# Performance work log

Hardware: AMD Instinct MI355X
Metric: run time of the kernel (lower is better)

The kernel has to match this reference:

```python
import jax, jax.numpy as jnp
import numpy as np

B = 128          # batch (stands in for bit-packed words)
C, H, W = 3, 32, 32
K = 64           # num_kernels
RFS, STRIDE = 5, 1
HO = (H - RFS) // STRIDE + 1   # 28
P = HO * HO                     # 784 output positions
G0 = 8                          # 2**tree_depth, tree_depth=3
NL1, NL2, NCLS = 64000, 32000, 10

# ALL_OPERATIONS order; each gate is multilinear: c0 + ca*a + cb*b + cab*a*b
COEF = jnp.array([
    [0, 0, 0, 0],    # zero
    [0, 0, 0, 1],    # and
    [0, 1, 0, -1],   # not_implies (a & ~b)
    [0, 1, 0, 0],    # a
    [0, 0, 1, -1],   # not_implied_by (b & ~a)
    [0, 0, 1, 0],    # b
    [0, 1, 1, -2],   # xor
    [0, 1, 1, -1],   # or
    [1, -1, -1, 1],  # not_or
    [1, -1, -1, 2],  # not_xor
    [1, 0, -1, 0],   # not_b
    [1, 0, -1, 1],   # implied_by (~b | a)
    [1, -1, 0, 0],   # not_a
    [1, -1, 0, 1],   # implies (~a | b)
    [1, 0, 0, -1],   # not_and
    [1, 0, 0, 0],    # one
], dtype=jnp.float32)


def _gate(a, b, ops):
    # ops: int array broadcastable against a/b trailing dims
    c = COEF[ops]  # [..., 4]
    return c[..., 0] + c[..., 1] * a + c[..., 2] * b + c[..., 3] * (a * b)


def _forward(x, cl, cr, o0, o1, o2, o3, a1, b1, p1, a2, b2, p2):
    # Conv logic layer: gather level-0 operand pairs -> [B, K, P, G0]
    la = jnp.take(x, cl, axis=1)
    lb = jnp.take(x, cr, axis=1)
    g = _gate(la, lb, o0[:, None, :])            # ops per (kernel, gate)
    # Binary tree reduction: level l pairs gates (2i, 2i+1)
    for ops in (o1, o2, o3):
        g = _gate(g[..., 0::2], g[..., 1::2], ops[:, None, :])
    z = g[..., 0].reshape(x.shape[0], K * P)     # [B, 50176]
    # Logic linear layers: out[i] = gate(in[a[i]], in[b[i]], op[i])
    z = _gate(z[:, a1], z[:, b1], p1)            # [B, NL1]
    z = _gate(z[:, a2], z[:, b2], p2)            # [B, NL2]
    # GroupSum: popcount per class group
    return z.reshape(z.shape[0], NCLS, -1).sum(-1)  # [B, 10]


def setup_inputs() -> dict:
    key = jax.random.key(0)
    x = (jax.random.uniform(key, (B, C * H * W)) < 0.5).astype(jnp.float32)
    rng = np.random.default_rng(0)
    bh = np.repeat(np.arange(HO), HO)  # h_pos per position
    bw = np.tile(np.arange(HO), HO)    # w_pos per position

    def conv_idx():
        dh = rng.integers(0, RFS, (K, P, G0))
        dw = rng.integers(0, RFS, (K, P, G0))
        dc = rng.integers(0, C, (K, P, G0))
        idx = dc * H * W + (bh[None, :, None] * STRIDE + dh) * W + (bw[None, :, None] * STRIDE + dw)
        return jnp.asarray(idx.astype(np.int32))

    ops = lambda shape: jnp.asarray(rng.integers(0, 16, shape).astype(np.int32))
    ridx = lambda hi, n: jnp.asarray(rng.integers(0, hi, n).astype(np.int32))
    return {
        'x': x,
        'conv_left_idx': conv_idx(), 'conv_right_idx': conv_idx(),
        'conv_ops0': ops((K, G0)), 'conv_ops1': ops((K, 4)),
        'conv_ops2': ops((K, 2)), 'conv_ops3': ops((K, 1)),
        'lin1_a': ridx(K * P, NL1), 'lin1_b': ridx(K * P, NL1), 'lin1_ops': ops((NL1,)),
        'lin2_a': ridx(NL1, NL2), 'lin2_b': ridx(NL1, NL2), 'lin2_ops': ops((NL2,)),
    }


def reference(x, conv_left_idx, conv_right_idx, conv_ops0, conv_ops1, conv_ops2, conv_ops3,
              lin1_a, lin1_b, lin1_ops, lin2_a, lin2_b, lin2_ops):
    return _forward(x, conv_left_idx, conv_right_idx, conv_ops0, conv_ops1, conv_ops2, conv_ops3,
                    lin1_a, lin1_b, lin1_ops, lin2_a, lin2_b, lin2_ops)
```

## Files before the change

### kernel.cpp

```cpp
#include <hip/hip_runtime.h>
#include <stdint.h>

#define NFEAT 3072
#define NWORD 2
#define NK 64
#define NP 784
#define NG 8
#define KP (NK * NP)
#define NL1 64000
#define NL2 32000
#define NCLS 10
#define NB 128
#define JBLK 128
#define CONV_THREADS 128

__device__ __forceinline__ uint64_t bsel64(uint64_t x, uint64_t p, uint64_t q) {
    return (x & p) | (~x & q);
}
__device__ __forceinline__ ulonglong2 gate128(ulonglong2 A, ulonglong2 B, int op) {
    uint64_t m3 = (uint64_t)0 - (uint64_t)((op >> 0) & 1);
    uint64_t m2 = (uint64_t)0 - (uint64_t)((op >> 1) & 1);
    uint64_t m1 = (uint64_t)0 - (uint64_t)((op >> 2) & 1);
    uint64_t m0 = (uint64_t)0 - (uint64_t)((op >> 3) & 1);
    ulonglong2 r;
    r.x = bsel64(A.x, bsel64(B.x, m3, m2), bsel64(B.x, m1, m0));
    r.y = bsel64(A.y, bsel64(B.y, m3, m2), bsel64(B.y, m1, m0));
    return r;
}

__global__ __launch_bounds__(256) void pack_kernel(const float* __restrict__ x,
                                                   uint64_t* __restrict__ xb,
                                                   float* __restrict__ out) {
    int gt = blockIdx.x * 256 + threadIdx.x;
    if (gt < NB * NCLS) out[gt] = 0.0f;
    int fw = gt >> 6;
    int lane = gt & 63;
    int f = fw >> 1, w = fw & 1;
    float val = x[(size_t)(w * 64 + lane) * NFEAT + f];
    uint64_t m = __ballot(val != 0.0f);
    if (lane == 0) xb[f * NWORD + w] = m;
}

__global__ __launch_bounds__(CONV_THREADS) void conv_kernel(
    const uint64_t* __restrict__ xb,
    const int* __restrict__ cl, const int* __restrict__ cr,
    const int* __restrict__ o0, const int* __restrict__ o1,
    const int* __restrict__ o2, const int* __restrict__ o3,
    uint64_t* __restrict__ z) {
    __shared__ uint64_t sxb[NFEAT * NWORD];
    {
        ulonglong2* s2 = reinterpret_cast<ulonglong2*>(sxb);
        const ulonglong2* g2 = reinterpret_cast<const ulonglong2*>(xb);
        for (int i = threadIdx.x; i < NFEAT; i += blockDim.x)
            s2[i] = g2[i];
    }
    __syncthreads();

    int t = blockIdx.x * CONV_THREADS + threadIdx.x;
    int k = t / NP;

    const int4* cl4 = reinterpret_cast<const int4*>(cl + (size_t)t * NG);
    const int4* cr4 = reinterpret_cast<const int4*>(cr + (size_t)t * NG);
    int4 l0 = cl4[0], l1 = cl4[1];
    int4 r0 = cr4[0], r1 = cr4[1];
    int la[NG] = {l0.x, l0.y, l0.z, l0.w, l1.x, l1.y, l1.z, l1.w};
    int rb[NG] = {r0.x, r0.y, r0.z, r0.w, r1.x, r1.y, r1.z, r1.w};

    int op0[NG], op1[4], op2[2], op3;
#pragma unroll
    for (int g = 0; g < NG; ++g) op0[g] = o0[k * NG + g];
#pragma unroll
    for (int g = 0; g < 4; ++g) op1[g] = o1[k * 4 + g];
#pragma unroll
    for (int g = 0; g < 2; ++g) op2[g] = o2[k * 2 + g];
    op3 = o3[k];

    const ulonglong2* sxb2 = reinterpret_cast<const ulonglong2*>(sxb);
    ulonglong2 gg[NG];
#pragma unroll
    for (int g = 0; g < NG; ++g) {
        ulonglong2 va = sxb2[la[g]];
        ulonglong2 vb = sxb2[rb[g]];
        gg[g] = gate128(va, vb, op0[g]);
    }
#pragma unroll
    for (int g = 0; g < 4; ++g)
        gg[g] = gate128(gg[2 * g], gg[2 * g + 1], op1[g]);
#pragma unroll
    for (int g = 0; g < 2; ++g)
        gg[g] = gate128(gg[2 * g], gg[2 * g + 1], op2[g]);
    reinterpret_cast<ulonglong2*>(z)[t] = gate128(gg[0], gg[1], op3);
}

__global__ __launch_bounds__(JBLK) void lin2_fused_kernel(
    const uint64_t* __restrict__ z,
    const int* __restrict__ a1, const int* __restrict__ b1,
    const int* __restrict__ p1,
    const int* __restrict__ a2, const int* __restrict__ b2,
    const int* __restrict__ p2, float* __restrict__ out) {
    __shared__ alignas(16) uint64_t s[NWORD][JBLK];
    int blk = blockIdx.x;
    const int chunks_per_cls = (NL2 / NCLS) / JBLK;
    int c = blk / chunks_per_cls;
    int j = c * (NL2 / NCLS) + (blk % chunks_per_cls) * JBLK + threadIdx.x;

    int ia = a2[j], ib = b2[j], op = p2[j];
    int iaa = a1[ia], iab = b1[ia], opa = p1[ia];
    int iba = a1[ib], ibb = b1[ib], opb = p1[ib];
    const ulonglong2* z2p = reinterpret_cast<const ulonglong2*>(z);
    ulonglong2 za = gate128(z2p[iaa], z2p[iab], opa);
    ulonglong2 zb = gate128(z2p[iba], z2p[ibb], opb);
    ulonglong2 zz = gate128(za, zb, op);
    s[0][threadIdx.x] = zz.x;
    s[1][threadIdx.x] = zz.y;
    __syncthreads();

    int bb = threadIdx.x;
    int w = bb >> 6, sh = bb & 63;
    const ulonglong2* sp = reinterpret_cast<const ulonglong2*>(s[w]);
    int cnt = 0;
#pragma unroll 16
    for (int jj = 0; jj < JBLK / 2; ++jj) {
        ulonglong2 v = sp[jj];
        cnt += (int)((v.x >> sh) & 1) + (int)((v.y >> sh) & 1);
    }
    atomicAdd(&out[bb * NCLS + c], (float)cnt);
}

extern "C" void kernel_launch(void* const* d_in, const int* in_sizes, int n_in,
                              void* d_out, int out_size, void* d_ws, size_t ws_size,
                              hipStream_t stream) {
    const float* x  = (const float*)d_in[0];
    const int* cl   = (const int*)d_in[1];
    const int* cr   = (const int*)d_in[2];
    const int* o0   = (const int*)d_in[3];
    const int* o1   = (const int*)d_in[4];
    const int* o2   = (const int*)d_in[5];
    const int* o3   = (const int*)d_in[6];
    const int* a1   = (const int*)d_in[7];
    const int* b1   = (const int*)d_in[8];
    const int* p1   = (const int*)d_in[9];
    const int* a2   = (const int*)d_in[10];
    const int* b2   = (const int*)d_in[11];
    const int* p2   = (const int*)d_in[12];
    float* out = (float*)d_out;

    uint8_t* ws = (uint8_t*)d_ws;
    uint64_t* xb = (uint64_t*)(ws);
    uint64_t* z  = (uint64_t*)(ws + 64 * 1024);

    pack_kernel<<<(NFEAT * NWORD * 64) / 256, 256, 0, stream>>>(x, xb, out);
    conv_kernel<<<KP / CONV_THREADS, CONV_THREADS, 0, stream>>>(xb, cl, cr, o0, o1, o2, o3, z);
    lin2_fused_kernel<<<NL2 / JBLK, JBLK, 0, stream>>>(z, a1, b1, p1, a2, b2, p2, out);
}
```

Measured before the change: 102.4 us.

## Fuse pack, conv and linear stages into one cooperative persistent kernel

```diff
diff --git a/kernel.cpp b/kernel.cpp
--- a/kernel.cpp
+++ b/kernel.cpp
@@ -1,5 +1,8 @@
 #include <hip/hip_runtime.h>
+#include <hip/hip_cooperative_groups.h>
 #include <stdint.h>
+
+namespace cg = cooperative_groups;
 
 #define NFEAT 3072
 #define NWORD 2
@@ -12,7 +15,9 @@
 #define NCLS 10
 #define NB 128
 #define JBLK 128
-#define CONV_THREADS 128
+#define GRID 256
+#define BLK 256
+#define ITEMS_PER_BLK (KP / GRID)
 
 __device__ __forceinline__ uint64_t bsel64(uint64_t x, uint64_t p, uint64_t q) {
     return (x & p) | (~x & q);
@@ -28,103 +33,112 @@
     return r;
 }
 
-__global__ __launch_bounds__(256) void pack_kernel(const float* __restrict__ x,
-                                                   uint64_t* __restrict__ xb,
-                                                   float* __restrict__ out) {
-    int gt = blockIdx.x * 256 + threadIdx.x;
-    if (gt < NB * NCLS) out[gt] = 0.0f;
-    int fw = gt >> 6;
-    int lane = gt & 63;
-    int f = fw >> 1, w = fw & 1;
-    float val = x[(size_t)(w * 64 + lane) * NFEAT + f];
-    uint64_t m = __ballot(val != 0.0f);
-    if (lane == 0) xb[f * NWORD + w] = m;
-}
-
-__global__ __launch_bounds__(CONV_THREADS) void conv_kernel(
-    const uint64_t* __restrict__ xb,
+__global__ __launch_bounds__(BLK) void fused_all(
+    const float* __restrict__ x,
     const int* __restrict__ cl, const int* __restrict__ cr,
     const int* __restrict__ o0, const int* __restrict__ o1,
     const int* __restrict__ o2, const int* __restrict__ o3,
-    uint64_t* __restrict__ z) {
-    __shared__ uint64_t sxb[NFEAT * NWORD];
+    const int* __restrict__ a1, const int* __restrict__ b1,
+    const int* __restrict__ p1,
+    const int* __restrict__ a2, const int* __restrict__ b2,
+    const int* __restrict__ p2,
+    uint64_t* __restrict__ xb, uint64_t* __restrict__ z,
+    float* __restrict__ out) {
+    __shared__ alignas(16) uint64_t sxb[NFEAT * NWORD];
+    cg::grid_group grid = cg::this_grid();
+
+    {
+        int gt = blockIdx.x * BLK + threadIdx.x;
+        if (gt < NB * NCLS) out[gt] = 0.0f;
+        int wave = gt >> 6;
+        int lane = gt & 63;
+#pragma unroll
+        for (int it = 0; it < (NFEAT * NWORD) / 1024; ++it) {
+            int task = wave + it * 1024;
+            int f = task >> 1, w = task & 1;
+            float val = x[(size_t)(w * 64 + lane) * NFEAT + f];
+            uint64_t m = __ballot(val != 0.0f);
+            if (lane == 0) xb[f * NWORD + w] = m;
+        }
+    }
+    grid.sync();
+
     {
         ulonglong2* s2 = reinterpret_cast<ulonglong2*>(sxb);
         const ulonglong2* g2 = reinterpret_cast<const ulonglong2*>(xb);
-        for (int i = threadIdx.x; i < NFEAT; i += blockDim.x)
+        for (int i = threadIdx.x; i < NFEAT; i += BLK)
             s2[i] = g2[i];
+        __syncthreads();
+
+        if (threadIdx.x < ITEMS_PER_BLK) {
+            int t = blockIdx.x * ITEMS_PER_BLK + threadIdx.x;
+            int k = t / NP;
+            const int4* cl4 = reinterpret_cast<const int4*>(cl + (size_t)t * NG);
+            const int4* cr4 = reinterpret_cast<const int4*>(cr + (size_t)t * NG);
+            int4 l0 = cl4[0], l1 = cl4[1];
+            int4 r0 = cr4[0], r1 = cr4[1];
+            int la[NG] = {l0.x, l0.y, l0.z, l0.w, l1.x, l1.y, l1.z, l1.w};
+            int rb[NG] = {r0.x, r0.y, r0.z, r0.w, r1.x, r1.y, r1.z, r1.w};
+            int op0[NG], op1[4], op2[2], op3;
+#pragma unroll
+            for (int g = 0; g < NG; ++g) op0[g] = o0[k * NG + g];
+#pragma unroll
+            for (int g = 0; g < 4; ++g) op1[g] = o1[k * 4 + g];
+#pragma unroll
+            for (int g = 0; g < 2; ++g) op2[g] = o2[k * 2 + g];
+            op3 = o3[k];
+
+            const ulonglong2* sxb2 = reinterpret_cast<const ulonglong2*>(sxb);
+            ulonglong2 gg[NG];
+#pragma unroll
+            for (int g = 0; g < NG; ++g)
+                gg[g] = gate128(sxb2[la[g]], sxb2[rb[g]], op0[g]);
+#pragma unroll
+            for (int g = 0; g < 4; ++g)
+                gg[g] = gate128(gg[2 * g], gg[2 * g + 1], op1[g]);
+#pragma unroll
+            for (int g = 0; g < 2; ++g)
+                gg[g] = gate128(gg[2 * g], gg[2 * g + 1], op2[g]);
+            reinterpret_cast<ulonglong2*>(z)[t] = gate128(gg[0], gg[1], op3);
+        }
     }
-    __syncthreads();
+    grid.sync();
 
-    int t = blockIdx.x * CONV_THREADS + threadIdx.x;
-    int k = t / NP;
+    if (blockIdx.x < (NL2 / JBLK)) {
+        ulonglong2* zs = reinterpret_cast<ulonglong2*>(sxb);
+        uint64_t* sbuf = sxb + 512;
+        const int chunks_per_cls = (NL2 / NCLS) / JBLK;
+        int c = blockIdx.x / chunks_per_cls;
+        int jbase = c * (NL2 / NCLS) + (blockIdx.x % chunks_per_cls) * JBLK;
 
-    const int4* cl4 = reinterpret_cast<const int4*>(cl + (size_t)t * NG);
-    const int4* cr4 = reinterpret_cast<const int4*>(cr + (size_t)t * NG);
-    int4 l0 = cl4[0], l1 = cl4[1];
-    int4 r0 = cr4[0], r1 = cr4[1];
-    int la[NG] = {l0.x, l0.y, l0.z, l0.w, l1.x, l1.y, l1.z, l1.w};
-    int rb[NG] = {r0.x, r0.y, r0.z, r0.w, r1.x, r1.y, r1.z, r1.w};
+        int u = threadIdx.x >> 1, role = threadIdx.x & 1;
+        int j = jbase + u;
+        int idx = role ? b2[j] : a2[j];
+        const ulonglong2* z2p = reinterpret_cast<const ulonglong2*>(z);
+        zs[threadIdx.x] = gate128(z2p[a1[idx]], z2p[b1[idx]], p1[idx]);
+        __syncthreads();
 
-    int op0[NG], op1[4], op2[2], op3;
+        if (threadIdx.x < JBLK) {
+            ulonglong2 r = gate128(zs[2 * threadIdx.x], zs[2 * threadIdx.x + 1],
+                                   p2[jbase + threadIdx.x]);
+            sbuf[threadIdx.x] = r.x;
+            sbuf[JBLK + threadIdx.x] = r.y;
+        }
+        __syncthreads();
+
+        int bb = threadIdx.x & 127;
+        int half = threadIdx.x >> 7;
+        int w = bb >> 6, sh = bb & 63;
+        const ulonglong2* sp = reinterpret_cast<const ulonglong2*>(sbuf + w * JBLK)
+                               + half * (JBLK / 4);
+        int cnt = 0;
 #pragma unroll
-    for (int g = 0; g < NG; ++g) op0[g] = o0[k * NG + g];
-#pragma unroll
-    for (int g = 0; g < 4; ++g) op1[g] = o1[k * 4 + g];
-#pragma unroll
-    for (int g = 0; g < 2; ++g) op2[g] = o2[k * 2 + g];
-    op3 = o3[k];
-
-    const ulonglong2* sxb2 = reinterpret_cast<const ulonglong2*>(sxb);
-    ulonglong2 gg[NG];
-#pragma unroll
-    for (int g = 0; g < NG; ++g) {
-        ulonglong2 va = sxb2[la[g]];
-        ulonglong2 vb = sxb2[rb[g]];
-        gg[g] = gate128(va, vb, op0[g]);
+        for (int jj = 0; jj < JBLK / 4; ++jj) {
+            ulonglong2 v = sp[jj];
+            cnt += (int)((v.x >> sh) & 1) + (int)((v.y >> sh) & 1);
+        }
+        atomicAdd(&out[bb * NCLS + c], (float)cnt);
     }
-#pragma unroll
-    for (int g = 0; g < 4; ++g)
-        gg[g] = gate128(gg[2 * g], gg[2 * g + 1], op1[g]);
-#pragma unroll
-    for (int g = 0; g < 2; ++g)
-        gg[g] = gate128(gg[2 * g], gg[2 * g + 1], op2[g]);
-    reinterpret_cast<ulonglong2*>(z)[t] = gate128(gg[0], gg[1], op3);
-}
-
-__global__ __launch_bounds__(JBLK) void lin2_fused_kernel(
-    const uint64_t* __restrict__ z,
-    const int* __restrict__ a1, const int* __restrict__ b1,
-    const int* __restrict__ p1,
-    const int* __restrict__ a2, const int* __restrict__ b2,
-    const int* __restrict__ p2, float* __restrict__ out) {
-    __shared__ alignas(16) uint64_t s[NWORD][JBLK];
-    int blk = blockIdx.x;
-    const int chunks_per_cls = (NL2 / NCLS) / JBLK;
-    int c = blk / chunks_per_cls;
-    int j = c * (NL2 / NCLS) + (blk % chunks_per_cls) * JBLK + threadIdx.x;
-
-    int ia = a2[j], ib = b2[j], op = p2[j];
-    int iaa = a1[ia], iab = b1[ia], opa = p1[ia];
-    int iba = a1[ib], ibb = b1[ib], opb = p1[ib];
-    const ulonglong2* z2p = reinterpret_cast<const ulonglong2*>(z);
-    ulonglong2 za = gate128(z2p[iaa], z2p[iab], opa);
-    ulonglong2 zb = gate128(z2p[iba], z2p[ibb], opb);
-    ulonglong2 zz = gate128(za, zb, op);
-    s[0][threadIdx.x] = zz.x;
-    s[1][threadIdx.x] = zz.y;
-    __syncthreads();
-
-    int bb = threadIdx.x;
-    int w = bb >> 6, sh = bb & 63;
-    const ulonglong2* sp = reinterpret_cast<const ulonglong2*>(s[w]);
-    int cnt = 0;
-#pragma unroll 16
-    for (int jj = 0; jj < JBLK / 2; ++jj) {
-        ulonglong2 v = sp[jj];
-        cnt += (int)((v.x >> sh) & 1) + (int)((v.y >> sh) & 1);
-    }
-    atomicAdd(&out[bb * NCLS + c], (float)cnt);
 }
 
 extern "C" void kernel_launch(void* const* d_in, const int* in_sizes, int n_in,
@@ -149,7 +163,9 @@
     uint64_t* xb = (uint64_t*)(ws);
     uint64_t* z  = (uint64_t*)(ws + 64 * 1024);
 
-    pack_kernel<<<(NFEAT * NWORD * 64) / 256, 256, 0, stream>>>(x, xb, out);
-    conv_kernel<<<KP / CONV_THREADS, CONV_THREADS, 0, stream>>>(xb, cl, cr, o0, o1, o2, o3, z);
-    lin2_fused_kernel<<<NL2 / JBLK, JBLK, 0, stream>>>(z, a1, b1, p1, a2, b2, p2, out);
+    void* args[] = {(void*)&x,  (void*)&cl, (void*)&cr, (void*)&o0, (void*)&o1,
+                    (void*)&o2, (void*)&o3, (void*)&a1, (void*)&b1, (void*)&p1,
+                    (void*)&a2, (void*)&b2, (void*)&p2, (void*)&xb, (void*)&z,
+                    (void*)&out};
+    hipLaunchCooperativeKernel(fused_all, dim3(GRID), dim3(BLK), args, 0, stream);
 }
```

Measured after the change: 176.2 us. 1.72x slower.
